# Performance work log

Hardware: AMD Instinct MI355X
Metric: run time of the kernel (lower is better)

Reference implementation:

```python
import jax, jax.numpy as jnp
import numpy as np
from jax import lax

N_STATES = 512
VOCAB = 32000
BATCH = 16
SEQ_LEN = 128


def setup_inputs() -> dict:
    key = jax.random.key(0)
    k_ids, k_em, k_tm, k_p = jax.random.split(key, 4)
    input_ids = jax.random.randint(k_ids, (BATCH, SEQ_LEN), 0, VOCAB, dtype=jnp.int64)
    em = jax.random.normal(k_em, (N_STATES, VOCAB), dtype=jnp.float32)
    tm = jax.random.normal(k_tm, (N_STATES, N_STATES), dtype=jnp.float32)
    p = jax.random.normal(k_p, (N_STATES,), dtype=jnp.float32)
    return {"input_ids": input_ids, "em": em, "tm": tm, "p": p}


def reference(input_ids, em, tm, p):
    """HMM forward algorithm in log space; returns mean NLL (scalar).

    em: [S, V] emission logits, tm: [S, S] transition logits, p: [S] prior logits.
    do_log_softmax=True -> normalize each in log space first.
    """
    log_em = jax.nn.log_softmax(em, axis=-1)   # [S, V]
    log_tm = jax.nn.log_softmax(tm, axis=-1)   # [S, S] rows = source state
    log_p = jax.nn.log_softmax(p, axis=-1)     # [S]

    # Gather emission log-probs per token: [B, T, S]
    em_tok = log_em.T[input_ids]

    # alpha_0[b, s] = log_p[s] + log_em[s, x_0]
    alpha0 = log_p[None, :] + em_tok[:, 0]     # [B, S]

    def step(alpha, e_t):
        # alpha: [B, S_src]; log-matmul: logsumexp over source states
        a = jax.nn.logsumexp(alpha[:, :, None] + log_tm[None, :, :], axis=1) + e_t
        return a, None

    em_rest = jnp.swapaxes(em_tok[:, 1:], 0, 1)  # [T-1, B, S]
    alpha_T, _ = lax.scan(step, alpha0, em_rest)

    # loss = -mean_b log p(x_b) = -mean_b logsumexp_s alpha_T[b, s]
    loss = -jnp.mean(jax.nn.logsumexp(alpha_T, axis=-1))
    return loss
```

## Files before the change

kernel.cpp:

```cpp
#include <hip/hip_runtime.h>
#include <hip/hip_bf16.h>

#define NS 512
#define NV 32000
#define NB 16
#define NT 128

#ifndef __has_builtin
#define __has_builtin(x) 0
#endif

typedef int v8i __attribute__((ext_vector_type(8)));
typedef float v4f __attribute__((ext_vector_type(4)));

__device__ inline unsigned enc_e4m3(float x) {
    x = fminf(x, 448.0f);
    unsigned u = __float_as_uint(x);
    if (x < 0.015625f) {
        return (unsigned)(int)rintf(x * 512.0f);
    }
    unsigned u2 = u + 0x7FFFFu + ((u >> 20) & 1u);
    return (((u2 >> 23) - 120u) << 3) | ((u2 >> 20) & 7u);
}

__device__ inline unsigned pack4_e4m3(float a, float b, float c, float d) {
#if __has_builtin(__builtin_amdgcn_cvt_pk_fp8_f32)
    int v = __builtin_amdgcn_cvt_pk_fp8_f32(a, b, 0, false);
    v = __builtin_amdgcn_cvt_pk_fp8_f32(c, d, v, true);
    return (unsigned)v;
#else
    return enc_e4m3(a) | (enc_e4m3(b) << 8) | (enc_e4m3(c) << 16) | (enc_e4m3(d) << 24);
#endif
}

#define DPPMAX(x, ctrl) \
    x = fmaxf(x, __int_as_float(__builtin_amdgcn_mov_dpp(__float_as_int(x), ctrl, 0xF, 0xF, true)))
#define DPPADD(x, ctrl) \
    x = x + __int_as_float(__builtin_amdgcn_mov_dpp(__float_as_int(x), ctrl, 0xF, 0xF, true))

__global__ __launch_bounds__(256) void k_emtok_T(
    const float* __restrict__ em, const int* __restrict__ ids,
    float* __restrict__ em_lin_T)
{
    const int s   = blockIdx.x;
    const int tid = threadIdx.x;
    const float* row = em + (size_t)s * NV;

    int idv[8];
#pragma unroll
    for (int k = 0; k < 8; ++k) idv[k] = ids[tid + 256 * k];
    float g[8];
#pragma unroll
    for (int k = 0; k < 8; ++k) g[k] = row[idv[k]];

    float sum = 0.f;
    const float4* row4 = (const float4*)row;
#pragma unroll 4
    for (int i = 0; i < 31; ++i) {
        float4 v = row4[tid + 256 * i];
        sum += __expf(v.x) + __expf(v.y) + __expf(v.z) + __expf(v.w);
    }
    sum += __expf(row[31744 + tid]);

#pragma unroll
    for (int off = 32; off; off >>= 1) sum += __shfl_down(sum, off);
    __shared__ float red[4];
    __shared__ float s_scale;
    if ((tid & 63) == 0) red[tid >> 6] = sum;
    __syncthreads();
    if (tid == 0) s_scale = (1.0f / ((red[0] + red[1]) + (red[2] + red[3]))) * 0x1p-18f;
    __syncthreads();
    const float scale = s_scale;

#pragma unroll
    for (int k = 0; k < 8; ++k)
        em_lin_T[(size_t)s * (NB * NT) + tid + 256 * k] = __expf(g[k]) * scale;
}

__global__ __launch_bounds__(256) void k_emtok_direct(
    const float* __restrict__ em, const int* __restrict__ ids,
    float* __restrict__ em_lin)
{
    const int s   = blockIdx.x;
    const int tid = threadIdx.x;
    const float* row = em + (size_t)s * NV;

    int idv[8];
#pragma unroll
    for (int k = 0; k < 8; ++k) idv[k] = ids[tid + 256 * k];
    float g[8];
#pragma unroll
    for (int k = 0; k < 8; ++k) g[k] = row[idv[k]];

    float sum = 0.f;
    const float4* row4 = (const float4*)row;
#pragma unroll 4
    for (int i = 0; i < 31; ++i) {
        float4 v = row4[tid + 256 * i];
        sum += __expf(v.x) + __expf(v.y) + __expf(v.z) + __expf(v.w);
    }
    sum += __expf(row[31744 + tid]);
#pragma unroll
    for (int off = 32; off; off >>= 1) sum += __shfl_down(sum, off);
    __shared__ float red[4];
    __shared__ float s_scale;
    if ((tid & 63) == 0) red[tid >> 6] = sum;
    __syncthreads();
    if (tid == 0) s_scale = (1.0f / ((red[0] + red[1]) + (red[2] + red[3]))) * 0x1p-18f;
    __syncthreads();
    const float scale = s_scale;
#pragma unroll
    for (int k = 0; k < 8; ++k)
        em_lin[(size_t)(tid + 256 * k) * NS + s] = __expf(g[k]) * scale;
}

__global__ __launch_bounds__(256) void k_tr(
    const float* __restrict__ emT, float* __restrict__ em_lin)
{
    __shared__ float tile[32][33];
    const int jb = blockIdx.x * 32;
    const int sb = blockIdx.y * 32;
    const int cc = threadIdx.x & 31;
    const int rr = threadIdx.x >> 5;
#pragma unroll
    for (int i = 0; i < 4; ++i) {
        int r = rr + 8 * i;
        tile[r][cc] = emT[(size_t)(sb + r) * (NB * NT) + jb + cc];
    }
    __syncthreads();
#pragma unroll
    for (int i = 0; i < 4; ++i) {
        int r = rr + 8 * i;
        em_lin[(size_t)(jb + r) * NS + sb + cc] = tile[cc][r];
    }
}

__global__ __launch_bounds__(64) void k_z(
    const float* __restrict__ tm, float* __restrict__ zscale)
{
    const int k    = blockIdx.x;
    const int lane = threadIdx.x;
    const float* row = tm + (size_t)k * NS;

    float4 a = ((const float4*)row)[lane * 2];
    float4 b = ((const float4*)row)[lane * 2 + 1];
    float sum = ((__expf(a.x) + __expf(a.y)) + (__expf(a.z) + __expf(a.w)))
              + ((__expf(b.x) + __expf(b.y)) + (__expf(b.z) + __expf(b.w)));
#pragma unroll
    for (int off = 32; off; off >>= 1) sum += __shfl_down(sum, off);
    if (lane == 0) zscale[k] = 1024.0f / sum;
}

__global__ __launch_bounds__(256) void k_pt2(
    const float* __restrict__ tm, const float* __restrict__ zscale,
    unsigned char* __restrict__ PT)
{
    __shared__ float tile[64][65];
    __shared__ float zs[64];
    const int kb  = blockIdx.x * 64;
    const int db  = blockIdx.y * 64;
    const int tid = threadIdx.x;
    const int c   = tid & 63;
    const int r0  = tid >> 6;

    if (tid < 64) zs[tid] = zscale[kb + tid];
#pragma unroll
    for (int i = 0; i < 16; ++i) {
        int r = r0 + 4 * i;
        tile[r][c] = tm[(size_t)(kb + r) * NS + db + c];
    }
    __syncthreads();

    const int d  = tid >> 2;
    const int ks = (tid & 3) * 16;
    unsigned px[4];
#pragma unroll
    for (int gq = 0; gq < 4; ++gq) {
        int k0 = ks + gq * 4;
        px[gq] = pack4_e4m3(__expf(tile[k0 + 0][d]) * zs[k0 + 0],
                            __expf(tile[k0 + 1][d]) * zs[k0 + 1],
                            __expf(tile[k0 + 2][d]) * zs[k0 + 2],
                            __expf(tile[k0 + 3][d]) * zs[k0 + 3]);
    }
    uint4 o; o.x = px[0]; o.y = px[1]; o.z = px[2]; o.w = px[3];
    *(uint4*)(PT + (size_t)(db + d) * NS + kb + ks) = o;
}

__global__ __launch_bounds__(512, 2) void k_scan(
    const float* __restrict__ em_lin, const unsigned char* __restrict__ PT,
    const float* __restrict__ p, float* __restrict__ out)
{
    const int tid = threadIdx.x;
    const int w   = tid >> 6;
    const int l   = tid & 63;
    const int lc  = l & 15;
    const int lq  = l >> 4;

    __shared__ unsigned int Ew[2][16 * 128];
    __shared__ unsigned int Stab[2][32];
    __shared__ float wm2[8][16];
    __shared__ float sbuf[16];

    v8i B[4][4];
#pragma unroll
    for (int nt = 0; nt < 4; ++nt) {
#pragma unroll
        for (int kt = 0; kt < 4; ++kt) {
            const uint4* src = (const uint4*)(PT + (size_t)((w * 4 + nt) * 16 + lc) * NS + kt * 128 + lq * 32);
            uint4 lo = src[0], hi = src[1];
            v8i bb;
            bb[0] = (int)lo.x; bb[1] = (int)lo.y; bb[2] = (int)lo.z; bb[3] = (int)lo.w;
            bb[4] = (int)hi.x; bb[5] = (int)hi.y; bb[6] = (int)hi.z; bb[7] = (int)hi.w;
            B[nt][kt] = bb;
        }
    }

    float zp = 0.f;
#pragma unroll
    for (int i = 0; i < 8; ++i) zp += __expf(p[l * 8 + i]);
    DPPADD(zp, 0x128); DPPADD(zp, 0x124); DPPADD(zp, 0xB1); DPPADD(zp, 0x4E);
    float Zp = __int_as_float(__builtin_amdgcn_readlane(__float_as_int(zp), 0))
             + __int_as_float(__builtin_amdgcn_readlane(__float_as_int(zp), 16))
             + __int_as_float(__builtin_amdgcn_readlane(__float_as_int(zp), 32))
             + __int_as_float(__builtin_amdgcn_readlane(__float_as_int(zp), 48));
    const float invZp = 1.0f / Zp;

    const int dbase0 = w * 64 + lc;

    float alpha[4][4];
#pragma unroll
    for (int nt = 0; nt < 4; ++nt) {
        float pl = __expf(p[dbase0 + 16 * nt]) * invZp;
#pragma unroll
        for (int r = 0; r < 4; ++r)
            alpha[nt][r] = pl * em_lin[(4 * lq + r) * (NT * NS) + dbase0 + 16 * nt];
    }

    int gsum = 0;
    const unsigned sel1 = (l & 1) ? 0x07030501u : 0x02060004u;
    const unsigned sel2 = (l & 2) ? 0x07060302u : 0x01000504u;
    const int mrow = 4 * lq + (l & 3);

    const float* ep[4];
#pragma unroll
    for (int r = 0; r < 4; ++r)
        ep[r] = em_lin + (size_t)(4 * lq + r) * (NT * NS) + NS + dbase0;

    int buf = 0;
    for (int t = 1; t < NT; ++t) {
        float epf[4][4];
#pragma unroll
        for (int nt = 0; nt < 4; ++nt)
#pragma unroll
            for (int r = 0; r < 4; ++r)
                epf[nt][r] = ep[r][16 * nt];
#pragma unroll
        for (int r = 0; r < 4; ++r) ep[r] += NS;

        unsigned byteS[4];
        float sc[4];
#pragma unroll
        for (int r = 0; r < 4; ++r) {
            float mx = fmaxf(fmaxf(alpha[0][r], alpha[1][r]), fmaxf(alpha[2][r], alpha[3][r]));
            DPPMAX(mx, 0x128); DPPMAX(mx, 0x124); DPPMAX(mx, 0xB1); DPPMAX(mx, 0x4E);
            unsigned eb = __float_as_uint(mx) >> 23;
            eb = eb < 7u ? 7u : (eb > 254u ? 254u : eb);
            byteS[r] = eb;
            sc[r] = __uint_as_float((261u - eb) << 23);
        }
        if (lc == 0)
            Stab[buf][w * 4 + lq] = byteS[0] | (byteS[1] << 8) | (byteS[2] << 16) | (byteS[3] << 24);

#pragma unroll
        for (int nt = 0; nt < 4; ++nt) {
            unsigned dw = pack4_e4m3(alpha[nt][0] * sc[0], alpha[nt][1] * sc[1],
                                     alpha[nt][2] * sc[2], alpha[nt][3] * sc[3]);
            int tmp = __builtin_amdgcn_mov_dpp((int)dw, 0xB1, 0xF, 0xF, true);
            dw = __builtin_amdgcn_perm(dw, (unsigned)tmp, sel1);
            tmp = __builtin_amdgcn_mov_dpp((int)dw, 0x4E, 0xF, 0xF, true);
            dw = __builtin_amdgcn_perm(dw, (unsigned)tmp, sel2);
            int chunk = ((w * 4 + nt) ^ mrow) & 31;
            Ew[buf][mrow * 128 + chunk * 4 + (lc >> 2)] = dw;
        }
        __syncthreads();

        const unsigned sh = (lc & 3) * 8;
        unsigned bS[8];
#pragma unroll
        for (int w2 = 0; w2 < 8; ++w2)
            bS[w2] = (Stab[buf][w2 * 4 + (lc >> 2)] >> sh) & 0xFFu;
        unsigned byteG = bS[0];
#pragma unroll
        for (int w2 = 1; w2 < 8; ++w2) byteG = byteG > bS[w2] ? byteG : bS[w2];
        gsum += (int)byteG - 126;

        int sA[4];
#pragma unroll
        for (int kt = 0; kt < 4; ++kt) {
            int sb = (int)bS[(kt * 4 + lq) >> 1] + 127 - (int)byteG;
            sb = sb < 0 ? 0 : sb;
            sA[kt] = sb * 0x01010101;
        }

        v8i A[4];
        const uint4* eb4 = (const uint4*)&Ew[buf][0];
#pragma unroll
        for (int kt = 0; kt < 4; ++kt) {
            uint4 lo = eb4[lc * 32 + (((kt * 8 + lq * 2 + 0) ^ lc) & 31)];
            uint4 hi = eb4[lc * 32 + (((kt * 8 + lq * 2 + 1) ^ lc) & 31)];
            v8i aa;
            aa[0] = (int)lo.x; aa[1] = (int)lo.y; aa[2] = (int)lo.z; aa[3] = (int)lo.w;
            aa[4] = (int)hi.x; aa[5] = (int)hi.y; aa[6] = (int)hi.z; aa[7] = (int)hi.w;
            A[kt] = aa;
        }

        v4f C[4];
#pragma unroll
        for (int nt = 0; nt < 4; ++nt) { C[nt][0] = 0.f; C[nt][1] = 0.f; C[nt][2] = 0.f; C[nt][3] = 0.f; }
#pragma unroll
        for (int kt = 0; kt < 4; ++kt)
#pragma unroll
            for (int nt = 0; nt < 4; ++nt)
                C[nt] = __builtin_amdgcn_mfma_scale_f32_16x16x128_f8f6f4(
                            A[kt], B[nt][kt], C[nt], 0, 0, 0, sA[kt], 0, 0x7F7F7F7F);

#pragma unroll
        for (int nt = 0; nt < 4; ++nt)
#pragma unroll
            for (int r = 0; r < 4; ++r)
                alpha[nt][r] = C[nt][r] * epf[nt][r];

        buf ^= 1;
    }

#pragma unroll
    for (int r = 0; r < 4; ++r) {
        float sm = ((alpha[0][r] + alpha[1][r]) + (alpha[2][r] + alpha[3][r]));
        DPPADD(sm, 0x128); DPPADD(sm, 0x124); DPPADD(sm, 0xB1); DPPADD(sm, 0x4E);
        if (lc == 0) wm2[w][4 * lq + r] = sm;
    }
    if (tid < 16) sbuf[tid] = (float)gsum;
    __syncthreads();
    if (w == 0) {
        const int li = l & 15;
        float s8 = 0.f;
#pragma unroll
        for (int j = 0; j < 8; ++j) s8 += wm2[j][li];
        float L2 = __log2f(s8) + 18.0f + sbuf[li];
        DPPADD(L2, 0x128); DPPADD(L2, 0x124); DPPADD(L2, 0xB1); DPPADD(L2, 0x4E);
        if (l == 0) out[0] = -(0.693147180559945f / 16.0f) * L2;
    }
}

extern "C" void kernel_launch(void* const* d_in, const int* in_sizes, int n_in,
                              void* d_out, int out_size, void* d_ws, size_t ws_size,
                              hipStream_t stream)
{
    const int*   ids = (const int*)d_in[0];
    const float* em  = (const float*)d_in[1];
    const float* tm  = (const float*)d_in[2];
    const float* p   = (const float*)d_in[3];
    float* out = (float*)d_out;

    float*          em_lin = (float*)d_ws;
    unsigned char*  PT     = (unsigned char*)d_ws + ((size_t)4 << 20);
    float*          zscale = (float*)((unsigned char*)d_ws + ((size_t)4 << 20) + ((size_t)256 << 10));
    float*          emT    = (float*)((unsigned char*)d_ws + ((size_t)4 << 20) + ((size_t)512 << 10));

    const bool big_ws = ws_size >= (((size_t)8 << 20) + ((size_t)512 << 10));

    if (big_ws) {
        k_emtok_T<<<NS, 256, 0, stream>>>(em, ids, emT);
        k_tr<<<dim3(64, 16), 256, 0, stream>>>(emT, em_lin);
    } else {
        k_emtok_direct<<<NS, 256, 0, stream>>>(em, ids, em_lin);
    }
    k_z<<<NS, 64, 0, stream>>>(tm, zscale);
    k_pt2<<<dim3(8, 8), 256, 0, stream>>>(tm, zscale, PT);
    k_scan<<<1, 512, 0, stream>>>(em_lin, PT, p, out);
}
```

Baseline: 295.5 us.

## Split HMM scan across four blocks, one batch row per MFMA quad

The single-block forward scan is split into four blocks, each handling four batch sequences. Each quad of lanes now carries one sequence, so only the first row of each MFMA A operand is populated and the other three rows are zero padding. Per-sequence scaling now uses a shared max exponent with an extra barrier per step instead of per-row MFMA scale bytes. Partial losses are combined with atomicAdd after a memset of the output, and the small-workspace fallback path is removed. The aim is to spread the latency-bound serial recurrence over more compute units, at the cost of wasted MFMA rows and an extra synchronisation each step.

```diff
diff --git a/kernel.cpp b/kernel.cpp
--- a/kernel.cpp
+++ b/kernel.cpp
@@ -77,43 +77,6 @@
         em_lin_T[(size_t)s * (NB * NT) + tid + 256 * k] = __expf(g[k]) * scale;
 }
 
-__global__ __launch_bounds__(256) void k_emtok_direct(
-    const float* __restrict__ em, const int* __restrict__ ids,
-    float* __restrict__ em_lin)
-{
-    const int s   = blockIdx.x;
-    const int tid = threadIdx.x;
-    const float* row = em + (size_t)s * NV;
-
-    int idv[8];
-#pragma unroll
-    for (int k = 0; k < 8; ++k) idv[k] = ids[tid + 256 * k];
-    float g[8];
-#pragma unroll
-    for (int k = 0; k < 8; ++k) g[k] = row[idv[k]];
-
-    float sum = 0.f;
-    const float4* row4 = (const float4*)row;
-#pragma unroll 4
-    for (int i = 0; i < 31; ++i) {
-        float4 v = row4[tid + 256 * i];
-        sum += __expf(v.x) + __expf(v.y) + __expf(v.z) + __expf(v.w);
-    }
-    sum += __expf(row[31744 + tid]);
-#pragma unroll
-    for (int off = 32; off; off >>= 1) sum += __shfl_down(sum, off);
-    __shared__ float red[4];
-    __shared__ float s_scale;
-    if ((tid & 63) == 0) red[tid >> 6] = sum;
-    __syncthreads();
-    if (tid == 0) s_scale = (1.0f / ((red[0] + red[1]) + (red[2] + red[3]))) * 0x1p-18f;
-    __syncthreads();
-    const float scale = s_scale;
-#pragma unroll
-    for (int k = 0; k < 8; ++k)
-        em_lin[(size_t)(tid + 256 * k) * NS + s] = __expf(g[k]) * scale;
-}
-
 __global__ __launch_bounds__(256) void k_tr(
     const float* __restrict__ emT, float* __restrict__ em_lin)
 {
@@ -190,16 +153,18 @@
     const float* __restrict__ em_lin, const unsigned char* __restrict__ PT,
     const float* __restrict__ p, float* __restrict__ out)
 {
+    const int bb  = blockIdx.x;
     const int tid = threadIdx.x;
     const int w   = tid >> 6;
     const int l   = tid & 63;
     const int lc  = l & 15;
     const int lq  = l >> 4;
 
-    __shared__ unsigned int Ew[2][16 * 128];
-    __shared__ unsigned int Stab[2][32];
-    __shared__ float wm2[8][16];
-    __shared__ float sbuf[16];
+    __shared__ unsigned Ew[16 * 128];
+    __shared__ unsigned wmE[8][4];
+    __shared__ unsigned mbuf[4];
+    __shared__ float    wm2[8][4];
+    __shared__ float    sbuf[4];
 
     v8i B[4][4];
 #pragma unroll
@@ -208,10 +173,10 @@
         for (int kt = 0; kt < 4; ++kt) {
             const uint4* src = (const uint4*)(PT + (size_t)((w * 4 + nt) * 16 + lc) * NS + kt * 128 + lq * 32);
             uint4 lo = src[0], hi = src[1];
-            v8i bb;
-            bb[0] = (int)lo.x; bb[1] = (int)lo.y; bb[2] = (int)lo.z; bb[3] = (int)lo.w;
-            bb[4] = (int)hi.x; bb[5] = (int)hi.y; bb[6] = (int)hi.z; bb[7] = (int)hi.w;
-            B[nt][kt] = bb;
+            v8i bb8;
+            bb8[0] = (int)lo.x; bb8[1] = (int)lo.y; bb8[2] = (int)lo.z; bb8[3] = (int)lo.w;
+            bb8[4] = (int)hi.x; bb8[5] = (int)hi.y; bb8[6] = (int)hi.z; bb8[7] = (int)hi.w;
+            B[nt][kt] = bb8;
         }
     }
 
@@ -226,88 +191,75 @@
     const float invZp = 1.0f / Zp;
 
     const int dbase0 = w * 64 + lc;
-
-    float alpha[4][4];
-#pragma unroll
-    for (int nt = 0; nt < 4; ++nt) {
-        float pl = __expf(p[dbase0 + 16 * nt]) * invZp;
-#pragma unroll
-        for (int r = 0; r < 4; ++r)
-            alpha[nt][r] = pl * em_lin[(4 * lq + r) * (NT * NS) + dbase0 + 16 * nt];
-    }
-
-    int gsum = 0;
+    const int gb     = bb * 4 + lq;
+
+    const float* epb0 = em_lin + (size_t)gb * (NT * NS) + dbase0;
+    float alpha[4];
+#pragma unroll
+    for (int nt = 0; nt < 4; ++nt)
+        alpha[nt] = __expf(p[dbase0 + 16 * nt]) * invZp * epb0[16 * nt];
+
+    int gsum = 18;
     const unsigned sel1 = (l & 1) ? 0x07030501u : 0x02060004u;
     const unsigned sel2 = (l & 2) ? 0x07060302u : 0x01000504u;
     const int mrow = 4 * lq + (l & 3);
 
-    const float* ep[4];
-#pragma unroll
-    for (int r = 0; r < 4; ++r)
-        ep[r] = em_lin + (size_t)(4 * lq + r) * (NT * NS) + NS + dbase0;
-
-    int buf = 0;
+    int aidx[8];
+#pragma unroll
+    for (int kt = 0; kt < 4; ++kt) {
+#pragma unroll
+        for (int c = 0; c < 2; ++c)
+            aidx[kt * 2 + c] = lc * 32 + (((kt * 8 + lq * 2 + c) ^ lc) & 31);
+    }
+    int widx[4];
+#pragma unroll
+    for (int nt = 0; nt < 4; ++nt)
+        widx[nt] = mrow * 128 + ((((w * 4 + nt) ^ mrow) & 31) << 2) + (lc >> 2);
+
+    const float* epb = epb0 + NS;
+
     for (int t = 1; t < NT; ++t) {
-        float epf[4][4];
-#pragma unroll
-        for (int nt = 0; nt < 4; ++nt)
-#pragma unroll
-            for (int r = 0; r < 4; ++r)
-                epf[nt][r] = ep[r][16 * nt];
-#pragma unroll
-        for (int r = 0; r < 4; ++r) ep[r] += NS;
-
-        unsigned byteS[4];
-        float sc[4];
-#pragma unroll
-        for (int r = 0; r < 4; ++r) {
-            float mx = fmaxf(fmaxf(alpha[0][r], alpha[1][r]), fmaxf(alpha[2][r], alpha[3][r]));
-            DPPMAX(mx, 0x128); DPPMAX(mx, 0x124); DPPMAX(mx, 0xB1); DPPMAX(mx, 0x4E);
-            unsigned eb = __float_as_uint(mx) >> 23;
-            eb = eb < 7u ? 7u : (eb > 254u ? 254u : eb);
-            byteS[r] = eb;
-            sc[r] = __uint_as_float((261u - eb) << 23);
+        float epf[4];
+#pragma unroll
+        for (int nt = 0; nt < 4; ++nt) epf[nt] = epb[16 * nt];
+        epb += NS;
+
+        float mx = fmaxf(fmaxf(alpha[0], alpha[1]), fmaxf(alpha[2], alpha[3]));
+        DPPMAX(mx, 0x128); DPPMAX(mx, 0x124); DPPMAX(mx, 0xB1); DPPMAX(mx, 0x4E);
+        if (lc == 0) wmE[w][lq] = __float_as_uint(mx) >> 23;
+        __syncthreads();
+
+        if (tid < 4) {
+            unsigned e0 = wmE[0][tid], e1 = wmE[1][tid], e2 = wmE[2][tid], e3 = wmE[3][tid];
+            unsigned e4 = wmE[4][tid], e5 = wmE[5][tid], e6 = wmE[6][tid], e7 = wmE[7][tid];
+            unsigned m01 = e0 > e1 ? e0 : e1,  m23 = e2 > e3 ? e2 : e3;
+            unsigned m45 = e4 > e5 ? e4 : e5,  m67 = e6 > e7 ? e6 : e7;
+            unsigned ma = m01 > m23 ? m01 : m23, mb = m45 > m67 ? m45 : m67;
+            mbuf[tid] = ma > mb ? ma : mb;
         }
-        if (lc == 0)
-            Stab[buf][w * 4 + lq] = byteS[0] | (byteS[1] << 8) | (byteS[2] << 16) | (byteS[3] << 24);
+        __syncthreads();
+
+        const unsigned eb = mbuf[lq];
+        const float sc = __uint_as_float((261u - eb) << 23);
+        gsum += (int)eb - 126;
 
 #pragma unroll
         for (int nt = 0; nt < 4; ++nt) {
-            unsigned dw = pack4_e4m3(alpha[nt][0] * sc[0], alpha[nt][1] * sc[1],
-                                     alpha[nt][2] * sc[2], alpha[nt][3] * sc[3]);
+            unsigned dw = pack4_e4m3(alpha[nt] * sc, 0.f, 0.f, 0.f);
             int tmp = __builtin_amdgcn_mov_dpp((int)dw, 0xB1, 0xF, 0xF, true);
             dw = __builtin_amdgcn_perm(dw, (unsigned)tmp, sel1);
             tmp = __builtin_amdgcn_mov_dpp((int)dw, 0x4E, 0xF, 0xF, true);
             dw = __builtin_amdgcn_perm(dw, (unsigned)tmp, sel2);
-            int chunk = ((w * 4 + nt) ^ mrow) & 31;
-            Ew[buf][mrow * 128 + chunk * 4 + (lc >> 2)] = dw;
+            Ew[widx[nt]] = dw;
         }
         __syncthreads();
 
-        const unsigned sh = (lc & 3) * 8;
-        unsigned bS[8];
-#pragma unroll
-        for (int w2 = 0; w2 < 8; ++w2)
-            bS[w2] = (Stab[buf][w2 * 4 + (lc >> 2)] >> sh) & 0xFFu;
-        unsigned byteG = bS[0];
-#pragma unroll
-        for (int w2 = 1; w2 < 8; ++w2) byteG = byteG > bS[w2] ? byteG : bS[w2];
-        gsum += (int)byteG - 126;
-
-        int sA[4];
+        v8i A[4];
+        const uint4* eb4 = (const uint4*)&Ew[0];
 #pragma unroll
         for (int kt = 0; kt < 4; ++kt) {
-            int sb = (int)bS[(kt * 4 + lq) >> 1] + 127 - (int)byteG;
-            sb = sb < 0 ? 0 : sb;
-            sA[kt] = sb * 0x01010101;
-        }
-
-        v8i A[4];
-        const uint4* eb4 = (const uint4*)&Ew[buf][0];
-#pragma unroll
-        for (int kt = 0; kt < 4; ++kt) {
-            uint4 lo = eb4[lc * 32 + (((kt * 8 + lq * 2 + 0) ^ lc) & 31)];
-            uint4 hi = eb4[lc * 32 + (((kt * 8 + lq * 2 + 1) ^ lc) & 31)];
+            uint4 lo = eb4[aidx[kt * 2 + 0]];
+            uint4 hi = eb4[aidx[kt * 2 + 1]];
             v8i aa;
             aa[0] = (int)lo.x; aa[1] = (int)lo.y; aa[2] = (int)lo.z; aa[3] = (int)lo.w;
             aa[4] = (int)hi.x; aa[5] = (int)hi.y; aa[6] = (int)hi.z; aa[7] = (int)hi.w;
@@ -322,33 +274,25 @@
 #pragma unroll
             for (int nt = 0; nt < 4; ++nt)
                 C[nt] = __builtin_amdgcn_mfma_scale_f32_16x16x128_f8f6f4(
-                            A[kt], B[nt][kt], C[nt], 0, 0, 0, sA[kt], 0, 0x7F7F7F7F);
+                            A[kt], B[nt][kt], C[nt], 0, 0, 0, 0x7F7F7F7F, 0, 0x7F7F7F7F);
 
 #pragma unroll
         for (int nt = 0; nt < 4; ++nt)
-#pragma unroll
-            for (int r = 0; r < 4; ++r)
-                alpha[nt][r] = C[nt][r] * epf[nt][r];
-
-        buf ^= 1;
-    }
-
-#pragma unroll
-    for (int r = 0; r < 4; ++r) {
-        float sm = ((alpha[0][r] + alpha[1][r]) + (alpha[2][r] + alpha[3][r]));
+            alpha[nt] = C[nt][0] * epf[nt];
+    }
+
+    {
+        float sm = (alpha[0] + alpha[1]) + (alpha[2] + alpha[3]);
         DPPADD(sm, 0x128); DPPADD(sm, 0x124); DPPADD(sm, 0xB1); DPPADD(sm, 0x4E);
-        if (lc == 0) wm2[w][4 * lq + r] = sm;
-    }
-    if (tid < 16) sbuf[tid] = (float)gsum;
-    __syncthreads();
-    if (w == 0) {
-        const int li = l & 15;
-        float s8 = 0.f;
-#pragma unroll
-        for (int j = 0; j < 8; ++j) s8 += wm2[j][li];
-        float L2 = __log2f(s8) + 18.0f + sbuf[li];
-        DPPADD(L2, 0x128); DPPADD(L2, 0x124); DPPADD(L2, 0xB1); DPPADD(L2, 0x4E);
-        if (l == 0) out[0] = -(0.693147180559945f / 16.0f) * L2;
+        if (lc == 0) wm2[w][lq] = sm;
+        if (w == 0 && lc == 0) sbuf[lq] = (float)gsum;
+    }
+    __syncthreads();
+    if (tid < 4) {
+        float s8 = ((wm2[0][tid] + wm2[1][tid]) + (wm2[2][tid] + wm2[3][tid]))
+                 + ((wm2[4][tid] + wm2[5][tid]) + (wm2[6][tid] + wm2[7][tid]));
+        float L2 = __log2f(s8) + sbuf[tid];
+        atomicAdd(out, -(0.693147180559945f / 16.0f) * L2);
     }
 }
 
@@ -367,15 +311,11 @@
     float*          zscale = (float*)((unsigned char*)d_ws + ((size_t)4 << 20) + ((size_t)256 << 10));
     float*          emT    = (float*)((unsigned char*)d_ws + ((size_t)4 << 20) + ((size_t)512 << 10));
 
-    const bool big_ws = ws_size >= (((size_t)8 << 20) + ((size_t)512 << 10));
-
-    if (big_ws) {
-        k_emtok_T<<<NS, 256, 0, stream>>>(em, ids, emT);
-        k_tr<<<dim3(64, 16), 256, 0, stream>>>(emT, em_lin);
-    } else {
-        k_emtok_direct<<<NS, 256, 0, stream>>>(em, ids, em_lin);
-    }
+    hipMemsetAsync(d_out, 0, sizeof(float), stream);
+
+    k_emtok_T<<<NS, 256, 0, stream>>>(em, ids, emT);
+    k_tr<<<dim3(64, 16), 256, 0, stream>>>(emT, em_lin);
     k_z<<<NS, 64, 0, stream>>>(tm, zscale);
     k_pt2<<<dim3(8, 8), 256, 0, stream>>>(tm, zscale, PT);
-    k_scan<<<1, 512, 0, stream>>>(em_lin, PT, p, out);
-}
+    k_scan<<<4, 512, 0, stream>>>(em_lin, PT, p, out);
+}
```

New measurement: 244.7 us. 1.21x faster.
